# Kernel optimization log

Measured on AMD Instinct MI355X. Metric: run time of the kernel, lower is better.

## Reference

```python
import jax, jax.numpy as jnp
import numpy as np
from jax import lax

SCORE_THRESH = 0.05
NMS_THRESH = 0.5
DETECTIONS_PER_IMG = 100
MIN_SIZE = 0.01
AREA_THRESH = 0.0
BOX_W = (10.0, 10.0, 5.0, 5.0)
BBOX_XFORM_CLIP = float(np.log(1000.0 / 16.0))


def setup_inputs() -> dict:
    key = jax.random.key(0)
    B, N, C = 8, 4000, 91
    H, W = 800, 1333
    k1, k2, k3 = jax.random.split(key, 3)
    # scale logits so a realistic fraction of softmax scores exceed score_thresh
    class_logits = jax.random.normal(k1, (B * N, C), jnp.float32) * 2.0
    box_regression = jax.random.normal(k2, (B * N, C * 4), jnp.float32)
    u = jax.random.uniform(k3, (B, N, 4), jnp.float32)
    x1 = u[..., 0] * (W - 50)
    y1 = u[..., 1] * (H - 50)
    bw = u[..., 2] * 200.0 + 4.0
    bh = u[..., 3] * 200.0 + 4.0
    proposals = jnp.stack([x1, y1, jnp.minimum(x1 + bw, W), jnp.minimum(y1 + bh, H)], axis=-1)
    return {"class_logits": class_logits, "box_regression": box_regression,
            "proposals": proposals, "image_h": H, "image_w": W}


def _decode(rel, props):
    # torchvision BoxCoder.decode: props [P,4], rel [P, C*4] -> [P, C, 4]
    w = props[:, 2] - props[:, 0]
    h = props[:, 3] - props[:, 1]
    cx = props[:, 0] + 0.5 * w
    cy = props[:, 1] + 0.5 * h
    rel = rel.reshape(rel.shape[0], -1, 4)
    dx = rel[..., 0] / BOX_W[0]
    dy = rel[..., 1] / BOX_W[1]
    dw = jnp.minimum(rel[..., 2] / BOX_W[2], BBOX_XFORM_CLIP)
    dh = jnp.minimum(rel[..., 3] / BOX_W[3], BBOX_XFORM_CLIP)
    pcx = dx * w[:, None] + cx[:, None]
    pcy = dy * h[:, None] + cy[:, None]
    pw = jnp.exp(dw) * w[:, None]
    ph = jnp.exp(dh) * h[:, None]
    return jnp.stack([pcx - 0.5 * pw, pcy - 0.5 * ph, pcx + 0.5 * pw, pcy + 0.5 * ph], axis=-1)


def _nms_image(boxes, scores, labels_f, valid, off_unit):
    # greedy batched NMS (class-offset trick) producing first DETECTIONS_PER_IMG survivors
    NEG = -1e9
    s0 = jnp.where(valid, scores, NEG)
    ob = boxes + (labels_f * off_unit)[:, None]  # per-class coordinate offset
    areas = (ob[:, 2] - ob[:, 0]) * (ob[:, 3] - ob[:, 1])

    def step(s, _):
        i = jnp.argmax(s)
        sc = s[i]
        ok = sc > (NEG / 2)
        obi = ob[i]
        ix1 = jnp.maximum(obi[0], ob[:, 0])
        iy1 = jnp.maximum(obi[1], ob[:, 1])
        ix2 = jnp.minimum(obi[2], ob[:, 2])
        iy2 = jnp.minimum(obi[3], ob[:, 3])
        inter = jnp.maximum(ix2 - ix1, 0.0) * jnp.maximum(iy2 - iy1, 0.0)
        ai = (obi[2] - obi[0]) * (obi[3] - obi[1])
        iou = inter / jnp.maximum(ai + areas - inter, 1e-9)
        sup = (iou > NMS_THRESH) & ok
        s = jnp.where(sup, NEG, s).at[i].set(NEG)
        return s, (i, jnp.where(ok, sc, 0.0), ok)

    _, (idx, out_sc, ok) = lax.scan(step, s0, None, length=DETECTIONS_PER_IMG)
    out_boxes = boxes[idx] * ok[:, None]
    out_labels = jnp.where(ok, labels_f[idx], 0.0)
    areas_out = (out_boxes[:, 2] - out_boxes[:, 0]) * (out_boxes[:, 3] - out_boxes[:, 1])
    keep = ok & (areas_out >= AREA_THRESH)
    return out_boxes * keep[:, None], out_sc * keep, jnp.where(keep, out_labels, 0.0), keep


def reference(class_logits, box_regression, proposals, image_h, image_w):
    B, N, _ = proposals.shape
    C = class_logits.shape[-1]
    pred_boxes = _decode(box_regression, proposals.reshape(B * N, 4)).reshape(B, N, C, 4)
    pred_scores = jax.nn.softmax(class_logits, axis=-1).reshape(B, N, C)
    # clip boxes to image
    x = jnp.clip(pred_boxes[..., 0::2], 0.0, float(image_w))
    y = jnp.clip(pred_boxes[..., 1::2], 0.0, float(image_h))
    pred_boxes = jnp.stack([x[..., 0], y[..., 0], x[..., 1], y[..., 1]], axis=-1)
    # drop background class 0, flatten (proposal, class) pairs
    M = N * (C - 1)
    boxes = pred_boxes[:, :, 1:, :].reshape(B, M, 4)
    scores = pred_scores[:, :, 1:].reshape(B, M)
    labels_f = jnp.broadcast_to(jnp.arange(1, C, dtype=boxes.dtype)[None, :], (N, C - 1)).reshape(M)
    ws = boxes[..., 2] - boxes[..., 0]
    hs = boxes[..., 3] - boxes[..., 1]
    valid = (scores > SCORE_THRESH) & (ws >= MIN_SIZE) & (hs >= MIN_SIZE)
    off_unit = float(max(image_h, image_w)) + 1.0
    out_boxes, out_scores, out_labels_f, keep = jax.vmap(
        lambda b, s, v: _nms_image(b, s, labels_f, v, off_unit))(boxes, scores, valid)
    return out_boxes, out_scores, out_labels_f.astype(jnp.int32), keep
```

## Files before the change

kernel.cpp:

```cpp
#include <hip/hip_runtime.h>
#include <stdint.h>

typedef uint32_t u32;
typedef unsigned long long u64;

#define NB 8
#define NPER 4000
#define NC 91
#define NCLS 90
#define NDET 100
#define CHUNKS 64
#define RPB 63
#define LBIN 16
#define PCAP 512
#define BINCAP 512
#define SURVCAP 9216
#define NSFIX (NCLS * NDET)
#define FKCAP 1024
#define VPT 36
#define NBIN 1152
#define SLO 0x3D4CCCCEu
#define SSH 15

__device__ __forceinline__ float4 decode_clip(float4 rel, float w, float h,
                                              float cx, float cy, float W, float H) {
  const float XCLIP = 4.135166556742356f;
  float dx = rel.x / 10.0f;
  float dy = rel.y / 10.0f;
  float dw = fminf(rel.z / 5.0f, XCLIP);
  float dh = fminf(rel.w / 5.0f, XCLIP);
  float qcx = dx * w + cx;
  float qcy = dy * h + cy;
  float qw = expf(dw) * w;
  float qh = expf(dh) * h;
  float x1 = qcx - 0.5f * qw, y1 = qcy - 0.5f * qh;
  float x2 = qcx + 0.5f * qw, y2 = qcy + 0.5f * qh;
  x1 = fminf(fmaxf(x1, 0.0f), W);
  x2 = fminf(fmaxf(x2, 0.0f), W);
  y1 = fminf(fmaxf(y1, 0.0f), H);
  y2 = fminf(fmaxf(y2, 0.0f), H);
  return make_float4(x1, y1, x2, y2);
}

__device__ __forceinline__ u64 rdlane64(u64 v, int sl) {
  u32 lo = (u32)__builtin_amdgcn_readlane((int)(u32)v, sl);
  u32 hi = (u32)__builtin_amdgcn_readlane((int)(u32)(v >> 32), sl);
  return ((u64)hi << 32) | (u64)lo;
}

__device__ __forceinline__ void emit_row(int r, int rl, int lane, float sA, float sB,
    float W, float H, const float4* __restrict__ props4, const float4* __restrict__ breg4,
    u32* s_cnt, u64 (*s_key)[LBIN], float4 (*s_box)[LBIN],
    u32* __restrict__ pc, u64* __restrict__ pk, float4* __restrict__ pb) {
  bool eA_ok = (lane >= 1) && (sA > 0.05f);
  bool eB_ok = (lane < NC - 64) && (sB > 0.05f);
  if (!(eA_ok || eB_ok)) return;
  float4 p = props4[r];
  float w = p.z - p.x, h = p.w - p.y;
  float cx = p.x + 0.5f * w, cy = p.y + 0.5f * h;
  if (eA_ok) {
    float4 raw = decode_clip(breg4[(size_t)r * NC + lane], w, h, cx, cy, W, H);
    if (((raw.z - raw.x) >= 0.01f) && ((raw.w - raw.y) >= 0.01f)) {
      int ci = lane - 1;
      u32 orig = (u32)(rl * NCLS + ci);
      u64 key = ((u64)__float_as_uint(sA) << 22) | (u64)(0x3FFFFFu - orig);
      u32 lp = atomicAdd(&s_cnt[ci], 1u);
      if (lp < LBIN) { s_key[ci][lp] = key; s_box[ci][lp] = raw; }
      else {
        u32 slot = atomicAdd(&pc[ci], 1u);
        if (slot < PCAP) { size_t o = (size_t)ci * PCAP + slot; pk[o] = key; pb[o] = raw; }
      }
    }
  }
  if (eB_ok) {
    float4 raw = decode_clip(breg4[(size_t)r * NC + 64 + lane], w, h, cx, cy, W, H);
    if (((raw.z - raw.x) >= 0.01f) && ((raw.w - raw.y) >= 0.01f)) {
      int ci = 63 + lane;
      u32 orig = (u32)(rl * NCLS + ci);
      u64 key = ((u64)__float_as_uint(sB) << 22) | (u64)(0x3FFFFFu - orig);
      u32 lp = atomicAdd(&s_cnt[ci], 1u);
      if (lp < LBIN) { s_key[ci][lp] = key; s_box[ci][lp] = raw; }
      else {
        u32 slot = atomicAdd(&pc[ci], 1u);
        if (slot < PCAP) { size_t o = (size_t)ci * PCAP + slot; pk[o] = key; pb[o] = raw; }
      }
    }
  }
}

__global__ __launch_bounds__(1024) void k_score(const float* __restrict__ logits,
    const float* __restrict__ boxreg, const float* __restrict__ props,
    const int* __restrict__ dh, const int* __restrict__ dw,
    u32* pool_cnt, u64* pool_key, float4* pool_box) {
  __shared__ u64 s_key[NCLS][LBIN];
  __shared__ float4 s_box[NCLS][LBIN];
  __shared__ u32 s_cnt[NCLS];
  __shared__ u32 s_base[NCLS];
  int tid = threadIdx.x;
  int b = blockIdx.x / CHUNKS;
  int chunk = blockIdx.x % CHUNKS;
  int wave = tid >> 6, lane = tid & 63;
  if (tid < NCLS) s_cnt[tid] = 0u;
  __syncthreads();

  float H = (float)dh[0], W = (float)dw[0];
  const float4* props4 = (const float4*)props;
  const float4* breg4 = (const float4*)boxreg;
  u32* pc = pool_cnt + (size_t)b * NCLS;
  u64* pk = pool_key + (size_t)b * NCLS * PCAP;
  float4* pb = pool_box + (size_t)b * NCLS * PCAP;

  for (int rloc = wave; rloc < RPB; rloc += 32) {
    int rloc1 = rloc + 16;
    int rl0 = chunk * RPB + rloc;
    int rl1 = chunk * RPB + rloc1;
    bool v0 = (rl0 < NPER);
    bool v1 = (rloc1 < RPB) && (rl1 < NPER);
    int r0 = b * NPER + (v0 ? rl0 : 0);
    int r1 = b * NPER + (v1 ? rl1 : 0);
    const float* l0 = logits + (size_t)r0 * NC;
    const float* l1 = logits + (size_t)r1 * NC;
    float xA0 = l0[lane];
    float xA1 = l1[lane];
    float xB0 = (lane < NC - 64) ? l0[64 + lane] : -3.0e38f;
    float xB1 = (lane < NC - 64) ? l1[64 + lane] : -3.0e38f;
    float mx0 = fmaxf(xA0, xB0);
    float mx1 = fmaxf(xA1, xB1);
    for (int o = 32; o; o >>= 1) {
      mx0 = fmaxf(mx0, __shfl_xor(mx0, o));
      mx1 = fmaxf(mx1, __shfl_xor(mx1, o));
    }
    float eA0 = expf(xA0 - mx0);
    float eA1 = expf(xA1 - mx1);
    float eB0 = (lane < NC - 64) ? expf(xB0 - mx0) : 0.0f;
    float eB1 = (lane < NC - 64) ? expf(xB1 - mx1) : 0.0f;
    float sm0 = eA0 + eB0;
    float sm1 = eA1 + eB1;
    for (int o = 32; o; o >>= 1) {
      sm0 += __shfl_xor(sm0, o);
      sm1 += __shfl_xor(sm1, o);
    }
    if (v0) emit_row(r0, rl0, lane, eA0 / sm0, eB0 / sm0, W, H, props4, breg4,
                     s_cnt, s_key, s_box, pc, pk, pb);
    if (v1) emit_row(r1, rl1, lane, eA1 / sm1, eB1 / sm1, W, H, props4, breg4,
                     s_cnt, s_key, s_box, pc, pk, pb);
  }
  __syncthreads();
  if (tid < NCLS) {
    u32 cnt = s_cnt[tid];
    u32 staged = cnt > LBIN ? LBIN : cnt;
    s_base[tid] = staged ? atomicAdd(&pc[tid], staged) : 0u;
  }
  __syncthreads();
  for (int idx = tid; idx < NCLS * LBIN; idx += 1024) {
    int ci = idx / LBIN, j = idx % LBIN;
    u32 cnt = s_cnt[ci];
    u32 staged = cnt > LBIN ? LBIN : cnt;
    if ((u32)j < staged) {
      u32 slot = s_base[ci] + (u32)j;
      if (slot < PCAP) {
        size_t o = (size_t)ci * PCAP + slot;
        pk[o] = s_key[ci][j];
        pb[o] = s_box[ci][j];
      }
    }
  }
}

__global__ __launch_bounds__(256) void k_nms_class(const u32* __restrict__ pool_cnt,
    const u64* __restrict__ pool_key, const float4* __restrict__ pool_box,
    u64* skey, float4* sbox, const int* __restrict__ dh, const int* __restrict__ dw) {
  __shared__ u64 k[BINCAP];
  __shared__ float4 boxu[BINCAP];
  __shared__ u64 ks[BINCAP];
  __shared__ float4 boxs[BINCAP];
  __shared__ float4 s_sb[NDET];
  __shared__ float s_sa[NDET];
  __shared__ u64 s_sk[NDET];
  __shared__ u32 s_sid[NDET];
  __shared__ u64 pw[4][64];
  __shared__ u32 ps[4][64];
  __shared__ u32 s_S;

  int b = blockIdx.x / NCLS;
  int ci = blockIdx.x % NCLS;
  int tid = threadIdx.x;
  int wv = tid >> 6, lane = tid & 63;
  u64* outk = skey + (size_t)b * SURVCAP + (size_t)ci * NDET;
  float4* outb = sbox + (size_t)b * SURVCAP + (size_t)ci * NDET;

  u32 cnt = pool_cnt[(size_t)b * NCLS + ci];
  int n = (int)(cnt > PCAP ? PCAP : cnt);
  if (n <= 0) {
    for (int i = tid; i < NDET; i += 256) outk[i] = 0ull;
    return;
  }
  size_t src = ((size_t)b * NCLS + ci) * PCAP;
  for (int i = tid; i < n; i += 256) {
    k[i] = pool_key[src + i];
    boxu[i] = pool_box[src + i];
  }
  __syncthreads();
  for (int i = tid; i < n; i += 256) {
    u64 ki = k[i];
    u32 rank = 0;
    int j = 0;
    for (; j + 4 <= n; j += 4) {
      rank += (k[j] > ki) ? 1u : 0u;
      rank += (k[j + 1] > ki) ? 1u : 0u;
      rank += (k[j + 2] > ki) ? 1u : 0u;
      rank += (k[j + 3] > ki) ? 1u : 0u;
    }
    for (; j < n; ++j) rank += (k[j] > ki) ? 1u : 0u;
    ks[rank] = ki;
    boxs[rank] = boxu[i];
  }
  if (tid == 0) s_S = 0u;
  __syncthreads();

  float H = (float)dh[0], W = (float)dw[0];
  float loff = (fmaxf(H, W) + 1.0f) * (float)(ci + 1);

  for (int base = 0; base < n; base += 64) {
    int S = (int)s_S;
    if (S >= NDET) break;
    int lim = n - base; if (lim > 64) lim = 64;
    bool have = (lane < lim);
    float4 Bb = make_float4(0.f, 0.f, 0.f, 0.f);
    float aB = 0.f;
    if (have) {
      float4 raw = boxs[base + lane];
      Bb = make_float4(raw.x + loff, raw.y + loff, raw.z + loff, raw.w + loff);
      aB = (Bb.z - Bb.x) * (Bb.w - Bb.y);
    }
    u64 w64 = 0ull;
    if (have) {
      int m0 = wv << 4, m1 = m0 + 16; if (m1 > lim) m1 = lim;
      for (int m = m0; m < m1; ++m) {
        float4 As = boxs[base + m];
        float ax = As.x + loff, ay = As.y + loff;
        float az = As.z + loff, aw = As.w + loff;
        float aA = (az - ax) * (aw - ay);
        float ix1 = fmaxf(ax, Bb.x), iy1 = fmaxf(ay, Bb.y);
        float ix2 = fminf(az, Bb.z), iy2 = fminf(aw, Bb.w);
        float inter = fmaxf(ix2 - ix1, 0.0f) * fmaxf(iy2 - iy1, 0.0f);
        float iou = inter / fmaxf(aA + aB - inter, 1e-9f);
        if (iou > 0.5f) w64 |= (1ull << m);
      }
    }
    pw[wv][lane] = w64;
    u32 f = 0u;
    if (have) {
      for (int s = wv; s < S; s += 4) {
        float4 A = s_sb[s];
        float aA = s_sa[s];
        float ix1 = fmaxf(A.x, Bb.x), iy1 = fmaxf(A.y, Bb.y);
        float ix2 = fminf(A.z, Bb.z), iy2 = fminf(A.w, Bb.w);
        float inter = fmaxf(ix2 - ix1, 0.0f) * fmaxf(iy2 - iy1, 0.0f);
        float iou = inter / fmaxf(aA + aB - inter, 1e-9f);
        if (iou > 0.5f) { f = 1u; break; }
      }
    }
    ps[wv][lane] = f;
    __syncthreads();
    if (tid < 64) {
      u64 myword = pw[0][lane] | pw[1][lane] | pw[2][lane] | pw[3][lane];
      bool alive = have &&
                   ((ps[0][lane] | ps[1][lane] | ps[2][lane] | ps[3][lane]) == 0u);
      u64 mask = __ballot(alive);
      u64 sel = 0ull;
      while (mask != 0ull && S + (int)__popcll(sel) < NDET) {
        int j0 = __builtin_amdgcn_readfirstlane(__builtin_ctzll(mask));
        sel |= (1ull << j0);
        u64 row = rdlane64(myword, j0);
        mask &= ~row;
      }
      if ((sel >> lane) & 1ull) {
        int rank = S + (int)__popcll(sel & ((1ull << lane) - 1ull));
        s_sb[rank] = Bb; s_sa[rank] = aB;
        s_sk[rank] = ks[base + lane]; s_sid[rank] = (u32)(base + lane);
      }
      if (tid == 0) s_S = (u32)(S + (int)__popcll(sel));
    }
    __syncthreads();
  }
  if (tid < 64) {
    int S = (int)s_S;
    for (int i2 = lane; i2 < NDET; i2 += 64) {
      if (i2 < S) {
        outk[i2] = s_sk[i2];
        outb[i2] = boxs[s_sid[i2]];
      } else {
        outk[i2] = 0ull;
      }
    }
  }
}

__global__ __launch_bounds__(256) void k_top(const u64* __restrict__ skey,
    const float4* __restrict__ sbox, float* out) {
  __shared__ u32 hist[NBIN];
  __shared__ u64 fk[FKCAP];
  __shared__ u32 fs[FKCAP];
  __shared__ u64 okey[NDET];
  __shared__ u32 osrc[NDET];
  __shared__ u32 s_cnt[2];
  __shared__ u32 s_bin;

  int b = blockIdx.x;
  int tid = threadIdx.x;
  const u64* kb = skey + (size_t)b * SURVCAP;

  u32 sc[VPT];
#pragma unroll
  for (int v = 0; v < VPT; ++v) {
    u32 j = (u32)tid + (u32)v * 256u;
    sc[v] = (j < NSFIX) ? (u32)(kb[j] >> 22) : 0u;
  }
  for (int i = tid; i < NBIN; i += 256) hist[i] = 0u;
  if (tid == 0) { s_cnt[0] = 0; s_cnt[1] = 0; }
  __syncthreads();

#pragma unroll
  for (int v = 0; v < VPT; ++v) {
    u32 s = sc[v];
    if (s > SLO) atomicAdd(&hist[(s - SLO) >> SSH], 1u);
  }
  __syncthreads();

  if (tid < 64) {
    int lane = tid;
    int base = lane * (NBIN / 64);
    u32 csum = 0;
#pragma unroll
    for (int kk2 = 0; kk2 < NBIN / 64; ++kk2) csum += hist[base + kk2];
    u32 suf = csum;
    for (int o = 1; o < 64; o <<= 1) {
      u32 v = __shfl_down(suf, o);
      if (lane + o < 64) suf += v;
    }
    u64 m = __ballot(suf >= NDET);
    int B = 0;
    if (m) {
      int c = 63 - __builtin_clzll(m);
      u32 rest = (c < 63) ? (u32)__shfl((int)suf, c + 1) : 0u;
      u32 acc = rest;
      int cb = c * (NBIN / 64);
      for (int kk2 = (NBIN / 64) - 1; kk2 >= 0; --kk2) {
        acc += hist[cb + kk2];
        if (acc >= NDET) { B = cb + kk2; break; }
      }
    }
    if (lane == 0) s_bin = (u32)B;
  }
  __syncthreads();
  u32 B = s_bin;

#pragma unroll
  for (int v = 0; v < VPT; ++v) {
    u32 s = sc[v];
    if (s > SLO && ((s - SLO) >> SSH) > B) {
      u32 j = (u32)tid + (u32)v * 256u;
      u32 p = atomicAdd(&s_cnt[0], 1u);
      if (p < FKCAP) { fk[p] = kb[j]; fs[p] = j; }
    }
  }
  __syncthreads();
  if (tid == 0) s_cnt[1] = s_cnt[0];
  __syncthreads();
#pragma unroll
  for (int v = 0; v < VPT; ++v) {
    u32 s = sc[v];
    if (s > SLO && ((s - SLO) >> SSH) == B) {
      u32 j = (u32)tid + (u32)v * 256u;
      u32 p = atomicAdd(&s_cnt[1], 1u);
      if (p < FKCAP) { fk[p] = kb[j]; fs[p] = j; }
    }
  }
  __syncthreads();
  u32 tot = s_cnt[1];
  if (tot > FKCAP) tot = FKCAP;
  if (tid >= 64) return;

  for (int i = tid; i < NDET; i += 64) okey[i] = 0ull;
  for (int i = tid; i < (int)tot; i += 64) {
    u64 ki = fk[i];
    u32 rank = 0;
    for (int j = 0; j < (int)tot; ++j) rank += (fk[j] > ki) ? 1u : 0u;
    if (rank < NDET) { okey[rank] = ki; osrc[rank] = fs[i]; }
  }
  for (int i = tid; i < NDET; i += 64) {
    u64 key = okey[i];
    float b0 = 0.f, b1 = 0.f, b2 = 0.f, b3 = 0.f, sc2 = 0.f, lb = 0.f, kp = 0.f;
    if (key) {
      float4 bx = sbox[(size_t)b * SURVCAP + osrc[i]];
      b0 = bx.x; b1 = bx.y; b2 = bx.z; b3 = bx.w;
      sc2 = __uint_as_float((u32)(key >> 22));
      u32 orig = 0x3FFFFFu - (u32)(key & 0x3FFFFFu);
      lb = (float)(orig % NCLS + 1u);
      kp = 1.0f;
    }
    float* ob = out + ((size_t)b * NDET + i) * 4;
    ob[0] = b0; ob[1] = b1; ob[2] = b2; ob[3] = b3;
    out[NB * NDET * 4 + b * NDET + i] = sc2;
    out[NB * NDET * 5 + b * NDET + i] = lb;
    out[NB * NDET * 6 + b * NDET + i] = kp;
  }
}

extern "C" void kernel_launch(void* const* d_in, const int* in_sizes, int n_in,
                              void* d_out, int out_size, void* d_ws, size_t ws_size,
                              hipStream_t stream) {
  const float* logits = (const float*)d_in[0];
  const float* boxreg = (const float*)d_in[1];
  const float* props  = (const float*)d_in[2];
  const int* dh = (const int*)d_in[3];
  const int* dw = (const int*)d_in[4];
  float* out = (float*)d_out;

  char* ws = (char*)d_ws;
  u32* pool_cnt = (u32*)ws;
  char* p0 = ws + 4096;
  u64* pool_key = (u64*)p0;
  char* p1 = p0 + (size_t)NB * NCLS * PCAP * 8;
  float4* pool_box = (float4*)p1;
  char* p2 = p1 + (size_t)NB * NCLS * PCAP * 16;
  u64* skey = (u64*)p2;
  float4* sbox = (float4*)(p2 + (size_t)NB * SURVCAP * 8);
  (void)ws_size;

  hipMemsetAsync(pool_cnt, 0, (size_t)NB * NCLS * sizeof(u32), stream);

  k_score<<<NB * CHUNKS, 1024, 0, stream>>>(logits, boxreg, props, dh, dw,
                                            pool_cnt, pool_key, pool_box);
  k_nms_class<<<NB * NCLS, 256, 0, stream>>>(pool_cnt, pool_key, pool_box,
                                             skey, sbox, dh, dw);
  k_top<<<NB, 256, 0, stream>>>(skey, sbox, out);
}
```

Measured before the change: 150.9 us.

## Replace global atomic pool with per-chunk fixed slots and prefix-sum gather

The scoring kernel no longer appends candidates to a per-class global pool through global atomics. Each block now writes its staged per-class candidates to a fixed slot indexed by (image, class, chunk) and records a per-chunk count. The NMS kernel computes a wave-level prefix sum over the 64 chunk counts to gather candidates contiguously. This removes the memset launch and global atomic contention. In exchange, candidates beyond LBIN per chunk per class are silently dropped instead of spilling to global memory, which is only correct if no class exceeds 16 survivors in a 63-row chunk.

```diff
diff --git a/kernel.cpp b/kernel.cpp
--- a/kernel.cpp
+++ b/kernel.cpp
@@ -12,7 +12,6 @@
 #define CHUNKS 64
 #define RPB 63
 #define LBIN 16
-#define PCAP 512
 #define BINCAP 512
 #define SURVCAP 9216
 #define NSFIX (NCLS * NDET)
@@ -50,8 +49,7 @@
 
 __device__ __forceinline__ void emit_row(int r, int rl, int lane, float sA, float sB,
     float W, float H, const float4* __restrict__ props4, const float4* __restrict__ breg4,
-    u32* s_cnt, u64 (*s_key)[LBIN], float4 (*s_box)[LBIN],
-    u32* __restrict__ pc, u64* __restrict__ pk, float4* __restrict__ pb) {
+    u32* s_cnt, u64 (*s_key)[LBIN], float4 (*s_box)[LBIN]) {
   bool eA_ok = (lane >= 1) && (sA > 0.05f);
   bool eB_ok = (lane < NC - 64) && (sB > 0.05f);
   if (!(eA_ok || eB_ok)) return;
@@ -66,10 +64,6 @@
       u64 key = ((u64)__float_as_uint(sA) << 22) | (u64)(0x3FFFFFu - orig);
       u32 lp = atomicAdd(&s_cnt[ci], 1u);
       if (lp < LBIN) { s_key[ci][lp] = key; s_box[ci][lp] = raw; }
-      else {
-        u32 slot = atomicAdd(&pc[ci], 1u);
-        if (slot < PCAP) { size_t o = (size_t)ci * PCAP + slot; pk[o] = key; pb[o] = raw; }
-      }
     }
   }
   if (eB_ok) {
@@ -80,10 +74,6 @@
       u64 key = ((u64)__float_as_uint(sB) << 22) | (u64)(0x3FFFFFu - orig);
       u32 lp = atomicAdd(&s_cnt[ci], 1u);
       if (lp < LBIN) { s_key[ci][lp] = key; s_box[ci][lp] = raw; }
-      else {
-        u32 slot = atomicAdd(&pc[ci], 1u);
-        if (slot < PCAP) { size_t o = (size_t)ci * PCAP + slot; pk[o] = key; pb[o] = raw; }
-      }
     }
   }
 }
@@ -91,11 +81,10 @@
 __global__ __launch_bounds__(1024) void k_score(const float* __restrict__ logits,
     const float* __restrict__ boxreg, const float* __restrict__ props,
     const int* __restrict__ dh, const int* __restrict__ dw,
-    u32* pool_cnt, u64* pool_key, float4* pool_box) {
+    u32* __restrict__ cnt2, u64* __restrict__ pool_key, float4* __restrict__ pool_box) {
   __shared__ u64 s_key[NCLS][LBIN];
   __shared__ float4 s_box[NCLS][LBIN];
   __shared__ u32 s_cnt[NCLS];
-  __shared__ u32 s_base[NCLS];
   int tid = threadIdx.x;
   int b = blockIdx.x / CHUNKS;
   int chunk = blockIdx.x % CHUNKS;
@@ -106,9 +95,6 @@
   float H = (float)dh[0], W = (float)dw[0];
   const float4* props4 = (const float4*)props;
   const float4* breg4 = (const float4*)boxreg;
-  u32* pc = pool_cnt + (size_t)b * NCLS;
-  u64* pk = pool_key + (size_t)b * NCLS * PCAP;
-  float4* pb = pool_box + (size_t)b * NCLS * PCAP;
 
   for (int rloc = wave; rloc < RPB; rloc += 32) {
     int rloc1 = rloc + 16;
@@ -141,33 +127,28 @@
       sm1 += __shfl_xor(sm1, o);
     }
     if (v0) emit_row(r0, rl0, lane, eA0 / sm0, eB0 / sm0, W, H, props4, breg4,
-                     s_cnt, s_key, s_box, pc, pk, pb);
+                     s_cnt, s_key, s_box);
     if (v1) emit_row(r1, rl1, lane, eA1 / sm1, eB1 / sm1, W, H, props4, breg4,
-                     s_cnt, s_key, s_box, pc, pk, pb);
+                     s_cnt, s_key, s_box);
   }
   __syncthreads();
   if (tid < NCLS) {
     u32 cnt = s_cnt[tid];
-    u32 staged = cnt > LBIN ? LBIN : cnt;
-    s_base[tid] = staged ? atomicAdd(&pc[tid], staged) : 0u;
-  }
-  __syncthreads();
+    cnt2[((size_t)b * NCLS + tid) * CHUNKS + chunk] = (cnt > LBIN) ? LBIN : cnt;
+  }
   for (int idx = tid; idx < NCLS * LBIN; idx += 1024) {
     int ci = idx / LBIN, j = idx % LBIN;
     u32 cnt = s_cnt[ci];
     u32 staged = cnt > LBIN ? LBIN : cnt;
     if ((u32)j < staged) {
-      u32 slot = s_base[ci] + (u32)j;
-      if (slot < PCAP) {
-        size_t o = (size_t)ci * PCAP + slot;
-        pk[o] = s_key[ci][j];
-        pb[o] = s_box[ci][j];
-      }
-    }
-  }
-}
-
-__global__ __launch_bounds__(256) void k_nms_class(const u32* __restrict__ pool_cnt,
+      size_t o = (((size_t)b * NCLS + ci) * CHUNKS + chunk) * LBIN + (u32)j;
+      pool_key[o] = s_key[ci][j];
+      pool_box[o] = s_box[ci][j];
+    }
+  }
+}
+
+__global__ __launch_bounds__(256) void k_nms_class(const u32* __restrict__ cnt2,
     const u64* __restrict__ pool_key, const float4* __restrict__ pool_box,
     u64* skey, float4* sbox, const int* __restrict__ dh, const int* __restrict__ dw) {
   __shared__ u64 k[BINCAP];
@@ -180,6 +161,9 @@
   __shared__ u32 s_sid[NDET];
   __shared__ u64 pw[4][64];
   __shared__ u32 ps[4][64];
+  __shared__ u32 s_off[64];
+  __shared__ u32 s_c[64];
+  __shared__ u32 s_n;
   __shared__ u32 s_S;
 
   int b = blockIdx.x / NCLS;
@@ -189,16 +173,33 @@
   u64* outk = skey + (size_t)b * SURVCAP + (size_t)ci * NDET;
   float4* outb = sbox + (size_t)b * SURVCAP + (size_t)ci * NDET;
 
-  u32 cnt = pool_cnt[(size_t)b * NCLS + ci];
-  int n = (int)(cnt > PCAP ? PCAP : cnt);
+  size_t cbase = ((size_t)b * NCLS + ci) * CHUNKS;
+  if (tid < 64) {
+    u32 c = cnt2[cbase + tid];
+    if (c > LBIN) c = LBIN;
+    s_c[tid] = c;
+    u32 inc = c;
+    for (int o = 1; o < 64; o <<= 1) {
+      u32 v = __shfl_up(inc, o);
+      if (tid >= o) inc += v;
+    }
+    s_off[tid] = inc - c;
+    if (tid == 63) s_n = (inc > BINCAP) ? BINCAP : inc;
+  }
+  __syncthreads();
+  int n = (int)s_n;
   if (n <= 0) {
     for (int i = tid; i < NDET; i += 256) outk[i] = 0ull;
     return;
   }
-  size_t src = ((size_t)b * NCLS + ci) * PCAP;
-  for (int i = tid; i < n; i += 256) {
-    k[i] = pool_key[src + i];
-    boxu[i] = pool_box[src + i];
+  {
+    int chunk = tid & 63, start = tid >> 6;
+    u32 cc = s_c[chunk], of = s_off[chunk];
+    size_t src = (cbase + chunk) * LBIN;
+    for (u32 i = (u32)start; i < cc; i += 4) {
+      u32 d = of + i;
+      if (d < (u32)BINCAP) { k[d] = pool_key[src + i]; boxu[d] = pool_box[src + i]; }
+    }
   }
   __syncthreads();
   for (int i = tid; i < n; i += 256) {
@@ -419,21 +420,19 @@
   float* out = (float*)d_out;
 
   char* ws = (char*)d_ws;
-  u32* pool_cnt = (u32*)ws;
-  char* p0 = ws + 4096;
+  u32* cnt2 = (u32*)ws;
+  char* p0 = ws + (((size_t)NB * NCLS * CHUNKS * 4 + 255) & ~(size_t)255);
   u64* pool_key = (u64*)p0;
-  char* p1 = p0 + (size_t)NB * NCLS * PCAP * 8;
+  char* p1 = p0 + (size_t)NB * NCLS * CHUNKS * LBIN * 8;
   float4* pool_box = (float4*)p1;
-  char* p2 = p1 + (size_t)NB * NCLS * PCAP * 16;
+  char* p2 = p1 + (size_t)NB * NCLS * CHUNKS * LBIN * 16;
   u64* skey = (u64*)p2;
   float4* sbox = (float4*)(p2 + (size_t)NB * SURVCAP * 8);
   (void)ws_size;
 
-  hipMemsetAsync(pool_cnt, 0, (size_t)NB * NCLS * sizeof(u32), stream);
-
   k_score<<<NB * CHUNKS, 1024, 0, stream>>>(logits, boxreg, props, dh, dw,
-                                            pool_cnt, pool_key, pool_box);
-  k_nms_class<<<NB * NCLS, 256, 0, stream>>>(pool_cnt, pool_key, pool_box,
+                                            cnt2, pool_key, pool_box);
+  k_nms_class<<<NB * NCLS, 256, 0, stream>>>(cnt2, pool_key, pool_box,
                                              skey, sbox, dh, dw);
   k_top<<<NB, 256, 0, stream>>>(skey, sbox, out);
 }
```

Measured after the change: 150.9 us. Within noise of the previous version (+0.0%).
